# Kernel tuning notes

Hardware: AMD Instinct MI355X
Metric: run time of the kernel (lower is better)

Reference implementation:

```python
import jax, jax.numpy as jnp
import numpy as np

N_USERS, N_ITEMS, EMB_DIM, N_INTENTS, N_EDGES, N_LAYERS = 50000, 100000, 64, 128, 3000000, 2
N_NODES = N_USERS + N_ITEMS


def _l2norm(x, eps=1e-8):
    # F.normalize(p=2, dim=-1, eps): x / max(||x||, eps)
    n = jnp.sqrt(jnp.sum(x * x, axis=-1, keepdims=True))
    return x / jnp.maximum(n, eps)


def setup_inputs() -> dict:
    key = jax.random.key(0)
    k0, k1, k2, k3, k4, k5 = jax.random.split(key, 6)
    xav_e = np.sqrt(2.0 / (N_NODES + EMB_DIM)).astype(np.float32)
    xav_i = np.sqrt(2.0 / (EMB_DIM + N_INTENTS)).astype(np.float32)
    return {
        "user_emb": jax.random.normal(k0, (N_USERS, EMB_DIM), jnp.float32) * xav_e,
        "item_emb": jax.random.normal(k1, (N_ITEMS, EMB_DIM), jnp.float32) * xav_e,
        "user_intent": jax.random.normal(k2, (EMB_DIM, N_INTENTS), jnp.float32) * xav_i,
        "item_intent": jax.random.normal(k3, (EMB_DIM, N_INTENTS), jnp.float32) * xav_i,
        "all_h": jax.random.randint(k4, (N_EDGES,), 0, N_NODES, jnp.int32),
        "all_t": jax.random.randint(k5, (N_EDGES,), 0, N_NODES, jnp.int32),
    }


def reference(user_emb, item_emb, user_intent, item_intent, all_h, all_t):
    E = all_h.shape[0]

    def spmm(vals, x):
        # y[h] += vals * x[t]  over edges  (torch_sparse.spmm)
        return jax.ops.segment_sum(vals[:, None] * x[all_t], all_h, num_segments=N_NODES)

    # _cal_sparse_adj: G = D^-1/2 A D^-1/2 on the unweighted edge list
    deg = jax.ops.segment_sum(jnp.ones((E,), jnp.float32), all_h, num_segments=N_NODES)
    d_inv_sqrt = jnp.where(deg > 0, deg, 1.0) ** -0.5 * (deg > 0)
    g_values = d_inv_sqrt[all_h] * d_inv_sqrt[all_t]

    def adaptive_values(src):
        # _adaptive_mask: cosine-sim edge weights, row-normalized
        he = _l2norm(src[all_h])
        te = _l2norm(src[all_t])
        edge_alpha = (jnp.sum(he * te, axis=1) + 1.0) * 0.5  # in [0,1]
        row_sum = jax.ops.segment_sum(edge_alpha, all_h, num_segments=N_NODES)
        d_inv = jnp.where(row_sum > 0, 1.0 / jnp.where(row_sum > 0, row_sum, 1.0), 0.0)
        return d_inv[all_h] * edge_alpha

    emb = jnp.concatenate([user_emb, item_emb], axis=0)  # [N, d]
    acc = emb
    for _ in range(N_LAYERS):
        gnn = spmm(g_values, emb)
        u, it = emb[:N_USERS], emb[N_USERS:]
        u_int = jax.nn.softmax(u @ user_intent, axis=1) @ user_intent.T
        i_int = jax.nn.softmax(it @ item_intent, axis=1) @ item_intent.T
        int_e = jnp.concatenate([u_int, i_int], axis=0)
        gaa = spmm(adaptive_values(gnn), emb)
        iaa = spmm(adaptive_values(int_e), emb)
        emb = gnn + int_e + gaa + iaa + emb
        acc = acc + emb
    # torch: sum over stacked layer embeddings == initial + each layer output
    return acc
```

## Files before the change

### kernel.cpp

```cpp
#include <hip/hip_runtime.h>
#include <hip/hip_bf16.h>

#define N_USERS   50000
#define N_ITEMS   100000
#define N_NODES   150000
#define DIM       64
#define N_INTENTS 128
#define N_EDGES   3000000
#define PSHIFT    9
#define PROWS     (1 << PSHIFT)
#define NPART     ((N_NODES + PROWS - 1) >> PSHIFT)
#define CHUNK     16384
#define NCHB      ((N_EDGES + CHUNK - 1) / CHUNK)

typedef __attribute__((ext_vector_type(8))) short short8v;
typedef __attribute__((ext_vector_type(4))) float f32x4;

static __device__ __forceinline__ float wsum64(float v){
#pragma unroll
  for (int m = 32; m >= 1; m >>= 1) v += __shfl_xor(v, m, 64);
  return v;
}
static __device__ __forceinline__ float wmax64(float v){
#pragma unroll
  for (int m = 32; m >= 1; m >>= 1) v = fmaxf(v, __shfl_xor(v, m, 64));
  return v;
}

template<int CTRL>
static __device__ __forceinline__ float dpp_ror_add(float x){
  int t = __builtin_amdgcn_update_dpp(0, __builtin_bit_cast(int, x),
                                      CTRL, 0xF, 0xF, true);
  return x + __builtin_bit_cast(float, t);
}
static __device__ __forceinline__ float row16_allsum(float x){
  x = dpp_ror_add<0x128>(x);
  x = dpp_ror_add<0x124>(x);
  x = dpp_ror_add<0x122>(x);
  x = dpp_ror_add<0x121>(x);
  return x;
}
template<int CTRL>
static __device__ __forceinline__ float dpp_ror_max(float x){
  int t = __builtin_amdgcn_update_dpp(0, __builtin_bit_cast(int, x),
                                      CTRL, 0xF, 0xF, true);
  return fmaxf(x, __builtin_bit_cast(float, t));
}
static __device__ __forceinline__ float row16_allmax(float x){
  x = dpp_ror_max<0x128>(x);
  x = dpp_ror_max<0x124>(x);
  x = dpp_ror_max<0x122>(x);
  x = dpp_ror_max<0x121>(x);
  return x;
}

static __device__ __forceinline__ unsigned short f2bf(float x){
  __hip_bfloat16 h = __float2bfloat16(x);
  return __builtin_bit_cast(unsigned short, h);
}
static __device__ __forceinline__ float bf_lo(unsigned int v){
  return __builtin_bit_cast(float, v << 16);
}
static __device__ __forceinline__ float bf_hi(unsigned int v){
  return __builtin_bit_cast(float, v & 0xFFFF0000u);
}
static __device__ __forceinline__ float bfval(unsigned short h){
  return __builtin_bit_cast(float, (unsigned int)h << 16);
}
static __device__ __forceinline__ void split2(float x, unsigned short& hi,
                                              unsigned short& lo){
  hi = f2bf(x);
  lo = f2bf(x - bfval(hi));
}

__global__ void k_init(const float* __restrict__ ue, const float* __restrict__ ie,
                       float* __restrict__ emb, float* __restrict__ acc,
                       unsigned short* __restrict__ embb){
  int i = blockIdx.x * 256 + threadIdx.x;
  if (i >= N_NODES * DIM) return;
  float v = (i < N_USERS * DIM) ? ue[i] : ie[i - N_USERS * DIM];
  emb[i] = v; acc[i] = v; embb[i] = f2bf(v);
}

__global__ void k_deg(const int* __restrict__ h, int* __restrict__ deg){
  int e = blockIdx.x * 256 + threadIdx.x;
  if (e < N_EDGES) atomicAdd(&deg[h[e]], 1);
}

__global__ void k_scan1(const int* __restrict__ deg, int* __restrict__ tmp,
                        int* __restrict__ aux){
  __shared__ int s[256];
  int t = threadIdx.x, i = blockIdx.x * 256 + t;
  int v = (i < N_NODES) ? deg[i] : 0;
  s[t] = v; __syncthreads();
  for (int off = 1; off < 256; off <<= 1){
    int x = (t >= off) ? s[t - off] : 0;
    __syncthreads();
    s[t] += x;
    __syncthreads();
  }
  if (i < N_NODES) tmp[i] = s[t];
  if (t == 255) aux[blockIdx.x] = s[255];
}

__global__ __launch_bounds__(1024) void k_scan2(int* __restrict__ aux, int n){
  __shared__ int s[1024];
  int t = threadIdx.x;
  int v = (t < n) ? aux[t] : 0;
  s[t] = v; __syncthreads();
  for (int off = 1; off < 1024; off <<= 1){
    int x = (t >= off) ? s[t - off] : 0;
    __syncthreads();
    s[t] += x;
    __syncthreads();
  }
  if (t < n) aux[t] = s[t] - v;
}

__global__ void k_rowptr(const int* __restrict__ tmp, const int* __restrict__ deg,
                         const int* __restrict__ aux, int* __restrict__ rp,
                         float* __restrict__ dis, int* __restrict__ gcur){
  int i = blockIdx.x * 256 + threadIdx.x;
  if (i < N_NODES){
    int v = aux[i >> 8] + tmp[i] - deg[i];
    rp[i] = v;
    int d = deg[i];
    dis[i] = (d > 0) ? (1.f / sqrtf((float)d)) : 0.f;
    if ((i & (PROWS - 1)) == 0) gcur[i >> PSHIFT] = v;
  }
  if (i == 0) rp[N_NODES] = N_EDGES;
}

__global__ __launch_bounds__(256) void k_part1(const int* __restrict__ h,
                                               const int* __restrict__ t,
                                               int* __restrict__ gcur,
                                               unsigned int* __restrict__ stg){
  __shared__ int hist[NPART];
  __shared__ int base[NPART];
  __shared__ int cnt2[NPART];
  int tid = threadIdx.x;
  int s = blockIdx.x * CHUNK;
  int e = min(s + CHUNK, N_EDGES);
  for (int p = tid; p < NPART; p += 256){ hist[p] = 0; cnt2[p] = 0; }
  __syncthreads();
  for (int i = s + tid; i < e; i += 256)
    atomicAdd(&hist[h[i] >> PSHIFT], 1);
  __syncthreads();
  for (int p = tid; p < NPART; p += 256){
    int c = hist[p];
    base[p] = c ? atomicAdd(&gcur[p], c) : 0;
  }
  __syncthreads();
  for (int i = s + tid; i < e; i += 256){
    int hh = h[i];
    int part = hh >> PSHIFT;
    int pos = base[part] + atomicAdd(&cnt2[part], 1);
    stg[pos] = ((unsigned)t[i] << PSHIFT) | (unsigned)(hh & (PROWS - 1));
  }
}

__global__ __launch_bounds__(256) void k_part2(const int* __restrict__ rp,
                                               const unsigned int* __restrict__ stg,
                                               int* __restrict__ t_csr){
  __shared__ int cur[PROWS];
  int b = blockIdx.x, tid = threadIdx.x;
  int row0 = b << PSHIFT;
  int rows = min(PROWS, N_NODES - row0);
  for (int i = tid; i < rows; i += 256) cur[i] = rp[row0 + i];
  __syncthreads();
  int s = rp[row0], e = rp[row0 + rows];
  for (int i = s + tid; i < e; i += 256){
    unsigned int v = stg[i];
    int pos = atomicAdd(&cur[v & (PROWS - 1)], 1);
    t_csr[pos] = (int)(v >> PSHIFT);
  }
}

__global__ void k_spmm_gnn(const int* __restrict__ rp, const int* __restrict__ t_csr,
                           const float* __restrict__ dis,
                           const uint2* __restrict__ embb2,
                           float* __restrict__ gnn, unsigned short* __restrict__ hgig_s){
  int w = (blockIdx.x * 256 + threadIdx.x) >> 6;
  int lane = threadIdx.x & 63;
  if (w >= N_NODES) return;
  int slot = lane >> 4, sub = lane & 15;
  int s = rp[w], e = rp[w + 1];
  float4 a = make_float4(0.f, 0.f, 0.f, 0.f);
  for (int i = s + slot; i < e; i += 4){
    int t = t_csr[i];
    float wt = dis[t];
    uint2 ev = embb2[t * 16 + sub];
    a.x = fmaf(wt, bf_lo(ev.x), a.x);
    a.y = fmaf(wt, bf_hi(ev.x), a.y);
    a.z = fmaf(wt, bf_lo(ev.y), a.z);
    a.w = fmaf(wt, bf_hi(ev.y), a.w);
  }
#pragma unroll
  for (int m = 16; m <= 32; m <<= 1){
    a.x += __shfl_xor(a.x, m, 64);
    a.y += __shfl_xor(a.y, m, 64);
    a.z += __shfl_xor(a.z, m, 64);
    a.w += __shfl_xor(a.w, m, 64);
  }
  float dw = dis[w];
  float4 gv = make_float4(dw * a.x, dw * a.y, dw * a.z, dw * a.w);
  float sq = gv.x * gv.x + gv.y * gv.y + gv.z * gv.z + gv.w * gv.w;
  float nrm = row16_allsum(sq);
  float invn = 1.f / fmaxf(sqrtf(nrm), 1e-8f);
  if (slot == 0){
    ((float4*)gnn)[w * 16 + sub] = gv;
    int base = (w * DIM + 4 * sub) * 2;
    hgig_s[base]     = f2bf(gv.x * invn);
    hgig_s[base + 2] = f2bf(gv.y * invn);
    hgig_s[base + 4] = f2bf(gv.z * invn);
    hgig_s[base + 6] = f2bf(gv.w * invn);
  }
}

__global__ void k_wprep(const float* __restrict__ wu, const float* __restrict__ wi,
                        unsigned short* __restrict__ wbuf){
  const float* W = blockIdx.x ? wi : wu;
  unsigned short* seg = wbuf + blockIdx.x * 32768;
  int tid = threadIdx.x;
  for (int i = tid; i < DIM * N_INTENTS; i += 256){
    unsigned short h, l; split2(W[i], h, l);
    seg[16384 + i] = h; seg[24576 + i] = l;
  }
  for (int idx = tid; idx < 16 * 64; idx += 256){
    int f = idx >> 6, lane = idx & 63;
    int nt = f >> 1, ks = f & 1, g = lane >> 4, c = lane & 15;
    int in = 16 * nt + c;
#pragma unroll
    for (int e = 0; e < 8; e++){
      int d = 8 * g + e + 32 * ks;
      unsigned short h, l; split2(W[d * N_INTENTS + in], h, l);
      seg[f * 512 + lane * 8 + e] = h;
      seg[8192 + f * 512 + lane * 8 + e] = l;
    }
  }
}

__global__ __launch_bounds__(256) void k_intent_mfma(
    const unsigned short* __restrict__ wseg, const float* __restrict__ emb,
    unsigned short* __restrict__ out_bf, unsigned short* __restrict__ hgig_s,
    int base_node, int count){
  __shared__ __align__(16) unsigned int Pl[4][2048];
  int wid = threadIdx.x >> 6, lane = threadIdx.x & 63;
  int tile = blockIdx.x * 4 + wid;
  if (tile * 16 >= count) return;
  int g = lane >> 4, c = lane & 15;

  const float4* erow = (const float4*)(emb + (size_t)(base_node + tile * 16 + c) * DIM);
  float4 ea0 = erow[2 * g],     eb0 = erow[2 * g + 1];
  float4 ea1 = erow[8 + 2 * g], eb1 = erow[9 + 2 * g];
  short8v ehi[2], elo[2];
  {
    float xs[16] = {ea0.x, ea0.y, ea0.z, ea0.w, eb0.x, eb0.y, eb0.z, eb0.w,
                    ea1.x, ea1.y, ea1.z, ea1.w, eb1.x, eb1.y, eb1.z, eb1.w};
#pragma unroll
    for (int ksi = 0; ksi < 2; ksi++)
#pragma unroll
      for (int e = 0; e < 8; e++){
        unsigned short h, l; split2(xs[ksi * 8 + e], h, l);
        ehi[ksi][e] = (short)h; elo[ksi][e] = (short)l;
      }
  }

  const uint4* w1hi = (const uint4*)wseg;
  const uint4* w1lo = (const uint4*)(wseg + 8192);
  f32x4 acc1[8];
#pragma unroll
  for (int nt = 0; nt < 8; nt++){
    f32x4 a = {0.f, 0.f, 0.f, 0.f};
#pragma unroll
    for (int ks = 0; ks < 2; ks++){
      short8v wh = __builtin_bit_cast(short8v, w1hi[(nt * 2 + ks) * 64 + lane]);
      short8v wl = __builtin_bit_cast(short8v, w1lo[(nt * 2 + ks) * 64 + lane]);
      a = __builtin_amdgcn_mfma_f32_16x16x32_bf16(ehi[ks], wh, a, 0, 0, 0);
      a = __builtin_amdgcn_mfma_f32_16x16x32_bf16(elo[ks], wh, a, 0, 0, 0);
      a = __builtin_amdgcn_mfma_f32_16x16x32_bf16(ehi[ks], wl, a, 0, 0, 0);
    }
    acc1[nt] = a;
  }

  unsigned int* pw = &Pl[wid][0];
#pragma unroll
  for (int r = 0; r < 4; r++){
    float m = acc1[0][r];
#pragma unroll
    for (int nt = 1; nt < 8; nt++) m = fmaxf(m, acc1[nt][r]);
    m = row16_allmax(m);
    float p[8];
    float s = 0.f;
#pragma unroll
    for (int nt = 0; nt < 8; nt++){ p[nt] = __expf(acc1[nt][r] - m); s += p[nt]; }
    s = row16_allsum(s);
    float inv = 1.f / s;
    int node = 4 * g + r;
    int swz = (node & 7) << 2;
    int base = node * 128 + c;
#pragma unroll
    for (int nt = 0; nt < 8; nt++){
      float v = p[nt] * inv;
      unsigned short h, l; split2(v, h, l);
      pw[(base + 16 * nt) ^ swz] = (unsigned int)h | ((unsigned int)l << 16);
    }
  }

  const uint4* pr = (const uint4*)pw;
  short8v phf[4], plf[4];
  int sw = (c & 7) << 2;
#pragma unroll
  for (int ks = 0; ks < 4; ks++){
    int i0 = c * 128 + 8 * g + 32 * ks;
    uint4 ra = pr[(i0 ^ sw) >> 2];
    uint4 rb = pr[((i0 + 4) ^ sw) >> 2];
    unsigned int q[8] = {ra.x, ra.y, ra.z, ra.w, rb.x, rb.y, rb.z, rb.w};
#pragma unroll
    for (int e = 0; e < 8; e++){
      phf[ks][e] = (short)(q[e] & 0xFFFFu);
      plf[ks][e] = (short)(q[e] >> 16);
    }
  }

  const uint4* w2hi = (const uint4*)(wseg + 16384);
  const uint4* w2lo = (const uint4*)(wseg + 24576);
  f32x4 acc2[4];
#pragma unroll
  for (int nt = 0; nt < 4; nt++){
    f32x4 a = {0.f, 0.f, 0.f, 0.f};
#pragma unroll
    for (int ks = 0; ks < 4; ks++){
      int fi = (16 * nt + c) * 16 + ks * 4 + g;
      short8v wh = __builtin_bit_cast(short8v, w2hi[fi]);
      short8v wl = __builtin_bit_cast(short8v, w2lo[fi]);
      a = __builtin_amdgcn_mfma_f32_16x16x32_bf16(phf[ks], wh, a, 0, 0, 0);
      a = __builtin_amdgcn_mfma_f32_16x16x32_bf16(plf[ks], wh, a, 0, 0, 0);
      a = __builtin_amdgcn_mfma_f32_16x16x32_bf16(phf[ks], wl, a, 0, 0, 0);
    }
    acc2[nt] = a;
  }

#pragma unroll
  for (int r = 0; r < 4; r++){
    float sq = 0.f;
#pragma unroll
    for (int nt = 0; nt < 4; nt++) sq = fmaf(acc2[nt][r], acc2[nt][r], sq);
    sq = row16_allsum(sq);
    float invn = 1.f / fmaxf(sqrtf(sq), 1e-8f);
    size_t gbase = (size_t)(base_node + tile * 16 + 4 * g + r) * DIM + c;
#pragma unroll
    for (int nt = 0; nt < 4; nt++){
      float v = acc2[nt][r];
      out_bf[gbase + 16 * nt] = f2bf(v);
      hgig_s[2 * (gbase + 16 * nt) + 1] = f2bf(v * invn);
    }
  }
}

__global__ void k_adafuse(const int* __restrict__ rp, const int* __restrict__ t_csr,
                          const uint4* __restrict__ hgig4,
                          const uint2* __restrict__ inte_bf2,
                          const uint2* __restrict__ embb2,
                          const float* __restrict__ emb,
                          float* __restrict__ gnn_io, float* __restrict__ acc,
                          uint2* __restrict__ embb_next2){
  int w = (blockIdx.x * 256 + threadIdx.x) >> 6;
  int lane = threadIdx.x & 63;
  if (w >= N_NODES) return;
  int slot = lane >> 4, sub = lane & 15;
  uint4 hp = hgig4[w * 16 + sub];
  float hg0 = bf_lo(hp.x), hg1 = bf_lo(hp.y), hg2 = bf_lo(hp.z), hg3 = bf_lo(hp.w);
  float hi0 = bf_hi(hp.x), hi1 = bf_hi(hp.y), hi2 = bf_hi(hp.z), hi3 = bf_hi(hp.w);
  int s = rp[w], e = rp[w + 1];
  float4 s1 = make_float4(0.f, 0.f, 0.f, 0.f);
  float4 s2 = make_float4(0.f, 0.f, 0.f, 0.f);
  float r1 = 0.f, r2 = 0.f;
  for (int i = s + slot; i < e; i += 4){
    int t = t_csr[i];
    uint4 tp = hgig4[t * 16 + sub];
    uint2 ev = embb2[t * 16 + sub];
    float p = hg0 * bf_lo(tp.x) + hg1 * bf_lo(tp.y)
            + hg2 * bf_lo(tp.z) + hg3 * bf_lo(tp.w);
    float q = hi0 * bf_hi(tp.x) + hi1 * bf_hi(tp.y)
            + hi2 * bf_hi(tp.z) + hi3 * bf_hi(tp.w);
    p = row16_allsum(p);
    q = row16_allsum(q);
    float a1 = fmaf(p, 0.5f, 0.5f);
    float a2 = fmaf(q, 0.5f, 0.5f);
    r1 += a1; r2 += a2;
    float v0 = bf_lo(ev.x), v1 = bf_hi(ev.x), v2 = bf_lo(ev.y), v3 = bf_hi(ev.y);
    s1.x = fmaf(a1, v0, s1.x); s1.y = fmaf(a1, v1, s1.y);
    s1.z = fmaf(a1, v2, s1.z); s1.w = fmaf(a1, v3, s1.w);
    s2.x = fmaf(a2, v0, s2.x); s2.y = fmaf(a2, v1, s2.y);
    s2.z = fmaf(a2, v2, s2.z); s2.w = fmaf(a2, v3, s2.w);
  }
#pragma unroll
  for (int m = 16; m <= 32; m <<= 1){
    s1.x += __shfl_xor(s1.x, m, 64); s1.y += __shfl_xor(s1.y, m, 64);
    s1.z += __shfl_xor(s1.z, m, 64); s1.w += __shfl_xor(s1.w, m, 64);
    s2.x += __shfl_xor(s2.x, m, 64); s2.y += __shfl_xor(s2.y, m, 64);
    s2.z += __shfl_xor(s2.z, m, 64); s2.w += __shfl_xor(s2.w, m, 64);
    r1   += __shfl_xor(r1,   m, 64); r2   += __shfl_xor(r2,   m, 64);
  }
  float d1 = (r1 > 0.f) ? 1.f / r1 : 0.f;
  float d2 = (r2 > 0.f) ? 1.f / r2 : 0.f;
  if (slot == 0){
    int idx4 = w * 16 + sub;
    float4 g = ((float4*)gnn_io)[idx4];
    uint2 it = inte_bf2[idx4];
    float4 em = ((const float4*)emb)[idx4];
    float4 nv;
    nv.x = g.x + bf_lo(it.x) + em.x + d1 * s1.x + d2 * s2.x;
    nv.y = g.y + bf_hi(it.x) + em.y + d1 * s1.y + d2 * s2.y;
    nv.z = g.z + bf_lo(it.y) + em.z + d1 * s1.z + d2 * s2.z;
    nv.w = g.w + bf_hi(it.y) + em.w + d1 * s1.w + d2 * s2.w;
    ((float4*)gnn_io)[idx4] = nv;
    float4 ac = ((float4*)acc)[idx4];
    ac.x += nv.x; ac.y += nv.y; ac.z += nv.z; ac.w += nv.w;
    ((float4*)acc)[idx4] = ac;
    uint2 ob;
    ob.x = (unsigned)f2bf(nv.x) | ((unsigned)f2bf(nv.y) << 16);
    ob.y = (unsigned)f2bf(nv.z) | ((unsigned)f2bf(nv.w) << 16);
    embb_next2[idx4] = ob;
  }
}

extern "C" void kernel_launch(void* const* d_in, const int* in_sizes, int n_in,
                              void* d_out, int out_size, void* d_ws, size_t ws_size,
                              hipStream_t stream){
  const float* ue = (const float*)d_in[0];
  const float* ie = (const float*)d_in[1];
  const float* wu = (const float*)d_in[2];
  const float* wi = (const float*)d_in[3];
  const int* all_h = (const int*)d_in[4];
  const int* all_t = (const int*)d_in[5];
  float* acc = (float*)d_out;

  char* p = (char*)d_ws;
  auto take = [&](size_t bytes)->char*{
    char* r = p; p += (bytes + 255) & ~size_t(255); return r;
  };
  float*  embA  = (float*)take(sizeof(float) * N_NODES * DIM);
  float*  embB  = (float*)take(sizeof(float) * N_NODES * DIM);
  unsigned int* hgig = (unsigned int*)take(sizeof(unsigned int) * N_NODES * DIM);
  unsigned short* inte_bf = (unsigned short*)take(sizeof(short) * N_NODES * DIM);
  unsigned short* embbA   = (unsigned short*)take(sizeof(short) * N_NODES * DIM);
  unsigned short* embbB   = (unsigned short*)take(sizeof(short) * N_NODES * DIM);
  unsigned short* wbuf    = (unsigned short*)take(sizeof(short) * 2 * 32768);
  int*    t_csr = (int*)take(sizeof(int) * N_EDGES);
  float*  dis   = (float*)take(sizeof(float) * N_NODES);
  int*    deg   = (int*)take(sizeof(int) * N_NODES);
  int*    tmp   = (int*)take(sizeof(int) * N_NODES);
  int*    aux   = (int*)take(sizeof(int) * 1024);
  int*    rp    = (int*)take(sizeof(int) * (N_NODES + 1));
  int*    gcur  = (int*)take(sizeof(int) * NPART);
  if ((size_t)(p - (char*)d_ws) > ws_size) return;
  unsigned int* stg = hgig;

  const int ELEM_B  = (N_NODES * DIM + 255) / 256;
  const int NODEW_B = (N_NODES * 64 + 255) / 256;
  const int EDGE_B  = (N_EDGES + 255) / 256;
  const int NODE_B  = (N_NODES + 255) / 256;

  hipMemsetAsync(deg, 0, sizeof(int) * N_NODES, stream);
  k_init<<<ELEM_B, 256, 0, stream>>>(ue, ie, embA, acc, embbA);
  k_wprep<<<2, 256, 0, stream>>>(wu, wi, wbuf);
  k_deg<<<EDGE_B, 256, 0, stream>>>(all_h, deg);
  k_scan1<<<NODE_B, 256, 0, stream>>>(deg, tmp, aux);
  k_scan2<<<1, 1024, 0, stream>>>(aux, NODE_B);
  k_rowptr<<<NODE_B, 256, 0, stream>>>(tmp, deg, aux, rp, dis, gcur);
  k_part1<<<NCHB, 256, 0, stream>>>(all_h, all_t, gcur, stg);
  k_part2<<<NPART, 256, 0, stream>>>(rp, stg, t_csr);

  const int UT_B = ((N_USERS / 16) + 3) / 4;
  const int IT_B = ((N_ITEMS / 16) + 3) / 4;

  float* eA = embA;
  float* eB = embB;
  unsigned short* ebA = embbA;
  unsigned short* ebB = embbB;
  for (int layer = 0; layer < 2; layer++){
    k_spmm_gnn<<<NODEW_B, 256, 0, stream>>>(rp, t_csr, dis, (const uint2*)ebA,
                                            eB, (unsigned short*)hgig);
    k_intent_mfma<<<UT_B, 256, 0, stream>>>(wbuf, eA, inte_bf,
                                            (unsigned short*)hgig, 0, N_USERS);
    k_intent_mfma<<<IT_B, 256, 0, stream>>>(wbuf + 32768, eA, inte_bf,
                                            (unsigned short*)hgig, N_USERS, N_ITEMS);
    k_adafuse<<<NODEW_B, 256, 0, stream>>>(rp, t_csr, (const uint4*)hgig,
                                           (const uint2*)inte_bf, (const uint2*)ebA,
                                           eA, eB, acc, (uint2*)ebB);
    float* t = eA; eA = eB; eB = t;
    unsigned short* tb = ebA; ebA = ebB; ebB = tb;
  }
}
```

Before: 1.067 ms.

## Use MFMA for edge cosine dot products and split normalized-embedding buffers

```diff
diff --git a/kernel.cpp b/kernel.cpp
--- a/kernel.cpp
+++ b/kernel.cpp
@@ -178,42 +178,48 @@
 
 __global__ void k_spmm_gnn(const int* __restrict__ rp, const int* __restrict__ t_csr,
                            const float* __restrict__ dis,
-                           const uint2* __restrict__ embb2,
-                           float* __restrict__ gnn, unsigned short* __restrict__ hgig_s){
+                           const unsigned short* __restrict__ embb,
+                           float* __restrict__ gnn, unsigned short* __restrict__ hgA){
   int w = (blockIdx.x * 256 + threadIdx.x) >> 6;
   int lane = threadIdx.x & 63;
   if (w >= N_NODES) return;
-  int slot = lane >> 4, sub = lane & 15;
+  int slot = lane >> 3, sub = lane & 7;
   int s = rp[w], e = rp[w + 1];
-  float4 a = make_float4(0.f, 0.f, 0.f, 0.f);
-  for (int i = s + slot; i < e; i += 4){
+  float a0=0.f,a1=0.f,a2=0.f,a3=0.f,a4=0.f,a5=0.f,a6=0.f,a7=0.f;
+  for (int i = s + slot; i < e; i += 8){
     int t = t_csr[i];
     float wt = dis[t];
-    uint2 ev = embb2[t * 16 + sub];
-    a.x = fmaf(wt, bf_lo(ev.x), a.x);
-    a.y = fmaf(wt, bf_hi(ev.x), a.y);
-    a.z = fmaf(wt, bf_lo(ev.y), a.z);
-    a.w = fmaf(wt, bf_hi(ev.y), a.w);
-  }
-#pragma unroll
-  for (int m = 16; m <= 32; m <<= 1){
-    a.x += __shfl_xor(a.x, m, 64);
-    a.y += __shfl_xor(a.y, m, 64);
-    a.z += __shfl_xor(a.z, m, 64);
-    a.w += __shfl_xor(a.w, m, 64);
+    uint4 ev = *(const uint4*)(embb + (size_t)t * 64 + 8 * sub);
+    a0 = fmaf(wt, bf_lo(ev.x), a0); a1 = fmaf(wt, bf_hi(ev.x), a1);
+    a2 = fmaf(wt, bf_lo(ev.y), a2); a3 = fmaf(wt, bf_hi(ev.y), a3);
+    a4 = fmaf(wt, bf_lo(ev.z), a4); a5 = fmaf(wt, bf_hi(ev.z), a5);
+    a6 = fmaf(wt, bf_lo(ev.w), a6); a7 = fmaf(wt, bf_hi(ev.w), a7);
+  }
+#pragma unroll
+  for (int m = 8; m <= 32; m <<= 1){
+    a0 += __shfl_xor(a0, m, 64); a1 += __shfl_xor(a1, m, 64);
+    a2 += __shfl_xor(a2, m, 64); a3 += __shfl_xor(a3, m, 64);
+    a4 += __shfl_xor(a4, m, 64); a5 += __shfl_xor(a5, m, 64);
+    a6 += __shfl_xor(a6, m, 64); a7 += __shfl_xor(a7, m, 64);
   }
   float dw = dis[w];
-  float4 gv = make_float4(dw * a.x, dw * a.y, dw * a.z, dw * a.w);
-  float sq = gv.x * gv.x + gv.y * gv.y + gv.z * gv.z + gv.w * gv.w;
-  float nrm = row16_allsum(sq);
-  float invn = 1.f / fmaxf(sqrtf(nrm), 1e-8f);
+  float g0 = dw*a0, g1 = dw*a1, g2 = dw*a2, g3 = dw*a3;
+  float g4 = dw*a4, g5 = dw*a5, g6 = dw*a6, g7 = dw*a7;
+  float sq = g0*g0 + g1*g1 + g2*g2 + g3*g3 + g4*g4 + g5*g5 + g6*g6 + g7*g7;
+#pragma unroll
+  for (int m = 1; m <= 4; m <<= 1) sq += __shfl_xor(sq, m, 64);
+  float invn = 1.f / fmaxf(sqrtf(sq), 1e-8f);
   if (slot == 0){
-    ((float4*)gnn)[w * 16 + sub] = gv;
-    int base = (w * DIM + 4 * sub) * 2;
-    hgig_s[base]     = f2bf(gv.x * invn);
-    hgig_s[base + 2] = f2bf(gv.y * invn);
-    hgig_s[base + 4] = f2bf(gv.z * invn);
-    hgig_s[base + 6] = f2bf(gv.w * invn);
+    float4 v0 = make_float4(g0, g1, g2, g3);
+    float4 v1 = make_float4(g4, g5, g6, g7);
+    ((float4*)gnn)[w * 16 + 2 * sub]     = v0;
+    ((float4*)gnn)[w * 16 + 2 * sub + 1] = v1;
+    uint4 ob;
+    ob.x = (unsigned)f2bf(g0*invn) | ((unsigned)f2bf(g1*invn) << 16);
+    ob.y = (unsigned)f2bf(g2*invn) | ((unsigned)f2bf(g3*invn) << 16);
+    ob.z = (unsigned)f2bf(g4*invn) | ((unsigned)f2bf(g5*invn) << 16);
+    ob.w = (unsigned)f2bf(g6*invn) | ((unsigned)f2bf(g7*invn) << 16);
+    *(uint4*)(hgA + (size_t)w * 64 + 8 * sub) = ob;
   }
 }
 
@@ -242,7 +248,7 @@
 
 __global__ __launch_bounds__(256) void k_intent_mfma(
     const unsigned short* __restrict__ wseg, const float* __restrict__ emb,
-    unsigned short* __restrict__ out_bf, unsigned short* __restrict__ hgig_s,
+    unsigned short* __restrict__ out_bf, unsigned short* __restrict__ hgB,
     int base_node, int count){
   __shared__ __align__(16) unsigned int Pl[4][2048];
   int wid = threadIdx.x >> 6, lane = threadIdx.x & 63;
@@ -353,47 +359,63 @@
     for (int nt = 0; nt < 4; nt++){
       float v = acc2[nt][r];
       out_bf[gbase + 16 * nt] = f2bf(v);
-      hgig_s[2 * (gbase + 16 * nt) + 1] = f2bf(v * invn);
+      hgB[gbase + 16 * nt] = f2bf(v * invn);
     }
   }
 }
 
 __global__ void k_adafuse(const int* __restrict__ rp, const int* __restrict__ t_csr,
-                          const uint4* __restrict__ hgig4,
+                          const unsigned short* __restrict__ hgA,
+                          const unsigned short* __restrict__ hgB,
                           const uint2* __restrict__ inte_bf2,
-                          const uint2* __restrict__ embb2,
+                          const unsigned short* __restrict__ embb,
                           const float* __restrict__ emb,
                           float* __restrict__ gnn_io, float* __restrict__ acc,
                           uint2* __restrict__ embb_next2){
   int w = (blockIdx.x * 256 + threadIdx.x) >> 6;
   int lane = threadIdx.x & 63;
   if (w >= N_NODES) return;
-  int slot = lane >> 4, sub = lane & 15;
-  uint4 hp = hgig4[w * 16 + sub];
-  float hg0 = bf_lo(hp.x), hg1 = bf_lo(hp.y), hg2 = bf_lo(hp.z), hg3 = bf_lo(hp.w);
-  float hi0 = bf_hi(hp.x), hi1 = bf_hi(hp.y), hi2 = bf_hi(hp.z), hi3 = bf_hi(hp.w);
+  int g = lane >> 4, c = lane & 15;
+  const unsigned short* wa = hgA + (size_t)w * 64;
+  const unsigned short* wb = hgB + (size_t)w * 64;
+  short8v bA0 = *(const short8v*)(wa + 8 * g);
+  short8v bA1 = *(const short8v*)(wa + 8 * g + 32);
+  short8v bB0 = *(const short8v*)(wb + 8 * g);
+  short8v bB1 = *(const short8v*)(wb + 8 * g + 32);
   int s = rp[w], e = rp[w + 1];
   float4 s1 = make_float4(0.f, 0.f, 0.f, 0.f);
   float4 s2 = make_float4(0.f, 0.f, 0.f, 0.f);
   float r1 = 0.f, r2 = 0.f;
-  for (int i = s + slot; i < e; i += 4){
-    int t = t_csr[i];
-    uint4 tp = hgig4[t * 16 + sub];
-    uint2 ev = embb2[t * 16 + sub];
-    float p = hg0 * bf_lo(tp.x) + hg1 * bf_lo(tp.y)
-            + hg2 * bf_lo(tp.z) + hg3 * bf_lo(tp.w);
-    float q = hi0 * bf_hi(tp.x) + hi1 * bf_hi(tp.y)
-            + hi2 * bf_hi(tp.z) + hi3 * bf_hi(tp.w);
-    p = row16_allsum(p);
-    q = row16_allsum(q);
-    float a1 = fmaf(p, 0.5f, 0.5f);
-    float a2 = fmaf(q, 0.5f, 0.5f);
-    r1 += a1; r2 += a2;
-    float v0 = bf_lo(ev.x), v1 = bf_hi(ev.x), v2 = bf_lo(ev.y), v3 = bf_hi(ev.y);
-    s1.x = fmaf(a1, v0, s1.x); s1.y = fmaf(a1, v1, s1.y);
-    s1.z = fmaf(a1, v2, s1.z); s1.w = fmaf(a1, v3, s1.w);
-    s2.x = fmaf(a2, v0, s2.x); s2.y = fmaf(a2, v1, s2.y);
-    s2.z = fmaf(a2, v2, s2.z); s2.w = fmaf(a2, v3, s2.w);
+  for (int i = s; i < e; i += 16){
+    int ia = i + c; if (ia >= e) ia = e - 1;
+    int t = t_csr[ia];
+    const unsigned short* ra = hgA + (size_t)t * 64;
+    const unsigned short* rb = hgB + (size_t)t * 64;
+    short8v aA0 = *(const short8v*)(ra + 8 * g);
+    short8v aA1 = *(const short8v*)(ra + 8 * g + 32);
+    short8v aB0 = *(const short8v*)(rb + 8 * g);
+    short8v aB1 = *(const short8v*)(rb + 8 * g + 32);
+    f32x4 p = {0.f, 0.f, 0.f, 0.f};
+    f32x4 q = {0.f, 0.f, 0.f, 0.f};
+    p = __builtin_amdgcn_mfma_f32_16x16x32_bf16(aA0, bA0, p, 0, 0, 0);
+    p = __builtin_amdgcn_mfma_f32_16x16x32_bf16(aA1, bA1, p, 0, 0, 0);
+    q = __builtin_amdgcn_mfma_f32_16x16x32_bf16(aB0, bB0, q, 0, 0, 0);
+    q = __builtin_amdgcn_mfma_f32_16x16x32_bf16(aB1, bB1, q, 0, 0, 0);
+#pragma unroll
+    for (int r = 0; r < 4; r++){
+      int ei = i + 4 * g + r;
+      bool valid = ei < e;
+      float a1v = valid ? fmaf(p[r], 0.5f, 0.5f) : 0.f;
+      float a2v = valid ? fmaf(q[r], 0.5f, 0.5f) : 0.f;
+      r1 += a1v; r2 += a2v;
+      int tt = t_csr[valid ? ei : (e - 1)];
+      uint2 ev = *(const uint2*)(embb + (size_t)tt * 64 + 4 * c);
+      float v0 = bf_lo(ev.x), v1 = bf_hi(ev.x), v2 = bf_lo(ev.y), v3 = bf_hi(ev.y);
+      s1.x = fmaf(a1v, v0, s1.x); s1.y = fmaf(a1v, v1, s1.y);
+      s1.z = fmaf(a1v, v2, s1.z); s1.w = fmaf(a1v, v3, s1.w);
+      s2.x = fmaf(a2v, v0, s2.x); s2.y = fmaf(a2v, v1, s2.y);
+      s2.z = fmaf(a2v, v2, s2.z); s2.w = fmaf(a2v, v3, s2.w);
+    }
   }
 #pragma unroll
   for (int m = 16; m <= 32; m <<= 1){
@@ -405,16 +427,16 @@
   }
   float d1 = (r1 > 0.f) ? 1.f / r1 : 0.f;
   float d2 = (r2 > 0.f) ? 1.f / r2 : 0.f;
-  if (slot == 0){
-    int idx4 = w * 16 + sub;
-    float4 g = ((float4*)gnn_io)[idx4];
+  if (g == 0){
+    int idx4 = w * 16 + c;
+    float4 gg = ((float4*)gnn_io)[idx4];
     uint2 it = inte_bf2[idx4];
     float4 em = ((const float4*)emb)[idx4];
     float4 nv;
-    nv.x = g.x + bf_lo(it.x) + em.x + d1 * s1.x + d2 * s2.x;
-    nv.y = g.y + bf_hi(it.x) + em.y + d1 * s1.y + d2 * s2.y;
-    nv.z = g.z + bf_lo(it.y) + em.z + d1 * s1.z + d2 * s2.z;
-    nv.w = g.w + bf_hi(it.y) + em.w + d1 * s1.w + d2 * s2.w;
+    nv.x = gg.x + bf_lo(it.x) + em.x + d1 * s1.x + d2 * s2.x;
+    nv.y = gg.y + bf_hi(it.x) + em.y + d1 * s1.y + d2 * s2.y;
+    nv.z = gg.z + bf_lo(it.y) + em.z + d1 * s1.z + d2 * s2.z;
+    nv.w = gg.w + bf_hi(it.y) + em.w + d1 * s1.w + d2 * s2.w;
     ((float4*)gnn_io)[idx4] = nv;
     float4 ac = ((float4*)acc)[idx4];
     ac.x += nv.x; ac.y += nv.y; ac.z += nv.z; ac.w += nv.w;
@@ -443,7 +465,8 @@
   };
   float*  embA  = (float*)take(sizeof(float) * N_NODES * DIM);
   float*  embB  = (float*)take(sizeof(float) * N_NODES * DIM);
-  unsigned int* hgig = (unsigned int*)take(sizeof(unsigned int) * N_NODES * DIM);
+  unsigned short* hgA = (unsigned short*)take(sizeof(short) * N_NODES * DIM);
+  unsigned short* hgB = (unsigned short*)take(sizeof(short) * N_NODES * DIM);
   unsigned short* inte_bf = (unsigned short*)take(sizeof(short) * N_NODES * DIM);
   unsigned short* embbA   = (unsigned short*)take(sizeof(short) * N_NODES * DIM);
   unsigned short* embbB   = (unsigned short*)take(sizeof(short) * N_NODES * DIM);
@@ -456,7 +479,7 @@
   int*    rp    = (int*)take(sizeof(int) * (N_NODES + 1));
   int*    gcur  = (int*)take(sizeof(int) * NPART);
   if ((size_t)(p - (char*)d_ws) > ws_size) return;
-  unsigned int* stg = hgig;
+  unsigned int* stg = (unsigned int*)hgA;
 
   const int ELEM_B  = (N_NODES * DIM + 255) / 256;
   const int NODEW_B = (N_NODES * 64 + 255) / 256;
@@ -481,14 +504,12 @@
   unsigned short* ebA = embbA;
   unsigned short* ebB = embbB;
   for (int layer = 0; layer < 2; layer++){
-    k_spmm_gnn<<<NODEW_B, 256, 0, stream>>>(rp, t_csr, dis, (const uint2*)ebA,
-                                            eB, (unsigned short*)hgig);
-    k_intent_mfma<<<UT_B, 256, 0, stream>>>(wbuf, eA, inte_bf,
-                                            (unsigned short*)hgig, 0, N_USERS);
-    k_intent_mfma<<<IT_B, 256, 0, stream>>>(wbuf + 32768, eA, inte_bf,
-                                            (unsigned short*)hgig, N_USERS, N_ITEMS);
-    k_adafuse<<<NODEW_B, 256, 0, stream>>>(rp, t_csr, (const uint4*)hgig,
-                                           (const uint2*)inte_bf, (const uint2*)ebA,
+    k_spmm_gnn<<<NODEW_B, 256, 0, stream>>>(rp, t_csr, dis, ebA, eB, hgA);
+    k_intent_mfma<<<UT_B, 256, 0, stream>>>(wbuf, eA, inte_bf, hgB, 0, N_USERS);
+    k_intent_mfma<<<IT_B, 256, 0, stream>>>(wbuf + 32768, eA, inte_bf, hgB,
+                                            N_USERS, N_ITEMS);
+    k_adafuse<<<NODEW_B, 256, 0, stream>>>(rp, t_csr, hgA, hgB,
+                                           (const uint2*)inte_bf, ebA,
                                            eA, eB, acc, (uint2*)ebB);
     float* t = eA; eA = eB; eB = t;
     unsigned short* tb = ebA; ebA = ebB; ebB = tb;
```

New measurement: 1.018 ms. 1.05x faster.
